# Kernel tuning notes

Measured on AMD Instinct MI355X. Metric: run time of the kernel, lower is better.

Reference implementation:

```python
import jax, jax.numpy as jnp
import numpy as np

B, V, D = 32768, 2, 512   # batch, views (code hard-codes 2 via cat(subject, subject)), hidden dim
S, L = 32, 8              # number of subjects, number of labels -> K = S*L groups
DENS_TEMP = 0.1           # args.Intersubsim_dens_temp (temperature/base_temperature are unused in forward)


def setup_inputs() -> dict:
    key = jax.random.key(0)
    k1, k2, k3 = jax.random.split(key, 3)
    X_data = jax.random.normal(k1, (B, V, D), dtype=jnp.float32)
    subject = jax.random.randint(k2, (B,), 0, S, dtype=jnp.int32)
    labels = jax.random.randint(k3, (B,), 0, L, dtype=jnp.int32)
    return {"X_data": X_data, "subject": subject, "labels": labels}


def reference(X_data, subject, labels):
    K = S * L
    # contrast_feature = cat(unbind(X_data, dim=1), dim=0): view-major stacking -> [V*B, D]
    feat = jnp.concatenate([X_data[:, v, :] for v in range(V)], axis=0)
    sub2 = jnp.concatenate([subject, subject])   # subject_ten
    lab2 = jnp.concatenate([labels, labels])     # labels_ten

    # group id per row; loop order (sorted unique subject, sorted unique label) == s*L + l
    gid = sub2 * L + lab2                         # [2B]
    counts = jax.ops.segment_sum(jnp.ones(gid.shape, feat.dtype), gid, K)   # [K]
    sums = jax.ops.segment_sum(feat, gid, K)                                 # [K, D]
    centroid = sums / counts[:, None]                                        # per-group mean

    # per-point euclidean distance to own-group centroid (torch.cdist)
    dist = jnp.sqrt(jnp.sum((feat - centroid[gid]) ** 2, axis=1))            # [2B]
    # density: mean(dist ** 0.5) / log(n_g + 10) for groups with >1 member
    mean_sqrt = jax.ops.segment_sum(jnp.sqrt(dist), gid, K) / counts
    dens = mean_sqrt / jnp.log(counts + 10.0)
    dmax = jnp.max(jnp.where(counts > 1, dens, -jnp.inf))
    density = jnp.where(counts > 1, dens, dmax)
    density = jnp.clip(density, jnp.quantile(density, 0.1), jnp.quantile(density, 0.9))
    density = DENS_TEMP * density / density.mean()
    # torch path goes through .tolist() -> density carries no gradient
    density = jax.lax.stop_gradient(density)

    # masks: positives = same label, different subject (group index equals raw id here)
    g_sub = jnp.arange(K, dtype=sub2.dtype) // L
    g_lab = jnp.arange(K, dtype=lab2.dtype) % L
    mask = ((sub2[:, None] != g_sub[None, :]) & (lab2[:, None] == g_lab[None, :])).astype(feat.dtype)  # [2B, K]
    # with S>=2 and all labels present, every row has at least one positive -> no row drop

    sim = (feat @ centroid.T) / density[None, :]          # [2B, K]
    sim = sim - jnp.max(sim, axis=1, keepdims=True)
    positive_sim = sim * mask
    # CrossEntropyLoss with soft (unnormalized) float targets: -sum target*log_softmax
    logp = jax.nn.log_softmax(positive_sim, axis=1)
    loss = -jnp.sum(mask * logp, axis=1) / jnp.sum(mask, axis=1)
    return loss.mean()
```

## Files before the change

### kernel.cpp

```cpp
#include <hip/hip_runtime.h>
#include <math.h>

#define BN 32768
#define DN 512
#define SN 32
#define LN 8
#define KN 256
#define N2 65536
#define SPLIT 8

typedef __attribute__((ext_vector_type(8))) short bf16x8;
typedef __attribute__((ext_vector_type(4))) float f32x4;

#define OFF_XBF     0ull
#define OFF_PART    67108864ull
#define OFF_SUMS    71303168ull
#define OFF_CENTB   71827456ull
#define OFF_GID     72089600ull
#define OFF_PERM    72220672ull
#define OFF_BASE    72351744ull
#define OFF_OFFW    72352772ull
#define OFF_COUNTS  72353796ull
#define OFF_SUMQ    72354820ull
#define OFF_INVD    72355844ull
#define OFF_LOSS    72356868ull
#define ZERO_OFF    OFF_COUNTS
#define ZERO_BYTES  (72356872ull - OFF_COUNTS)

__device__ __forceinline__ float atomAddF(float* p, float v) {
  return unsafeAtomicAdd(p, v);
}

__device__ __forceinline__ ushort f2bf(float x) {
  union { float f; unsigned u; } v; v.f = x;
  unsigned u = v.u;
  unsigned r = (u + 0x7fffu + ((u >> 16) & 1u)) >> 16;
  return (ushort)r;
}

__device__ __forceinline__ float bf2f(ushort x) {
  union { unsigned u; float f; } v; v.u = ((unsigned)x) << 16;
  return v.f;
}

__global__ __launch_bounds__(256) void k0_gid(const int* __restrict__ subject,
    const int* __restrict__ labels, int* __restrict__ gid, int* __restrict__ counts) {
  __shared__ int hist[KN];
  hist[threadIdx.x] = 0;
  __syncthreads();
  const int b0 = blockIdx.x * 1024;
  for (int i = threadIdx.x; i < 1024; i += 256) {
    int b = b0 + i;
    int g = subject[b] * LN + labels[b];
    gid[b] = g;
    atomicAdd(&hist[g], 1);
  }
  __syncthreads();
  if (hist[threadIdx.x]) atomicAdd(&counts[threadIdx.x], 2 * hist[threadIdx.x]);
}

__global__ __launch_bounds__(256) void k0b_scan(const int* __restrict__ counts,
    int* __restrict__ base, int* __restrict__ offw) {
  __shared__ int sh[KN];
  const int t = threadIdx.x;
  const int h = counts[t] >> 1;
  sh[t] = h;
  __syncthreads();
  for (int d = 1; d < 256; d <<= 1) {
    int add = (t >= d) ? sh[t - d] : 0;
    __syncthreads();
    sh[t] += add;
    __syncthreads();
  }
  const int excl = sh[t] - h;
  base[t] = excl;
  offw[t] = excl;
  if (t == 255) base[256] = sh[255];
}

__global__ __launch_bounds__(256) void k0c_scatter(const int* __restrict__ gid,
    int* __restrict__ offw, int* __restrict__ perm) {
  const int b = blockIdx.x * 256 + threadIdx.x;
  const int g = gid[b];
  const int pos = atomicAdd(&offw[g], 1);
  perm[pos] = b;
}

__global__ __launch_bounds__(256) void k1_sums(const float* __restrict__ X,
    const int* __restrict__ perm, const int* __restrict__ base,
    ushort* __restrict__ Xb, float* __restrict__ partial) {
  __shared__ float buf[512];
  const int g = blockIdx.x >> 3;
  const int s = blockIdx.x & (SPLIT - 1);
  const int t = threadIdx.x;
  const int start = base[g], end = base[g + 1];

  float4 acc = {0.f, 0.f, 0.f, 0.f};
  int i = start + s;
  if (i < end) {
    int idx = perm[i];
    float4 x = *(const float4*)(X + (size_t)idx * 1024 + t * 4);
    while (true) {
      const int inext = i + SPLIT;
      int idxn = idx;
      float4 xn = x;
      if (inext < end) {
        idxn = perm[inext];
        xn = *(const float4*)(X + (size_t)idxn * 1024 + t * 4);
      }
      acc.x += x.x; acc.y += x.y; acc.z += x.z; acc.w += x.w;
      ushort4 u = {f2bf(x.x), f2bf(x.y), f2bf(x.z), f2bf(x.w)};
      const size_t dst = (t < 128) ? ((size_t)idx * DN + t * 4)
                                   : ((size_t)(idx + BN) * DN + (t - 128) * 4);
      *(ushort4*)(Xb + dst) = u;
      if (inext >= end) break;
      i = inext; idx = idxn; x = xn;
    }
  }
  if (t >= 128) *(float4*)&buf[(t - 128) * 4] = acc;
  __syncthreads();
  if (t < 128) {
    float4 o = *(float4*)&buf[t * 4];
    float4 out = {acc.x + o.x, acc.y + o.y, acc.z + o.z, acc.w + o.w};
    *(float4*)&partial[((size_t)s * KN + g) * DN + t * 4] = out;
  }
}

__global__ __launch_bounds__(256) void k1b_cent(const float* __restrict__ partial,
    const int* __restrict__ counts, float* __restrict__ sums,
    ushort* __restrict__ centB) {
  const int i = blockIdx.x * 256 + threadIdx.x;
  const int g = i >> 9;
  float ss = 0.f;
#pragma unroll
  for (int s = 0; s < SPLIT; ++s) ss += partial[(size_t)s * (KN * DN) + i];
  sums[i] = ss;
  centB[i] = f2bf(ss / (float)counts[g]);
}

__global__ __launch_bounds__(256) void k3_dist(const ushort* __restrict__ Xb,
    const int* __restrict__ perm, const int* __restrict__ base,
    const float* __restrict__ sums, const int* __restrict__ counts,
    float* __restrict__ sumq) {
  __shared__ float wacc[4];
  const int g = blockIdx.x >> 3;
  const int s = blockIdx.x & (SPLIT - 1);
  const int t = threadIdx.x;
  const int w = t >> 6;
  const int lane = t & 63;
  const int start = base[g], end = base[g + 1];
  const int nviews = 2 * (end - start);
  const float invc = 1.0f / (float)counts[g];
  const float* sp = sums + g * DN + lane * 8;
  float4 c0 = *(const float4*)sp;
  float4 c1 = *(const float4*)(sp + 4);
  const float cs[8] = {c0.x * invc, c0.y * invc, c0.z * invc, c0.w * invc,
                       c1.x * invc, c1.y * invc, c1.z * invc, c1.w * invc};
  float q = 0.f;
  const int vs = s * 4 + w;
  for (int j = vs; j < nviews; j += SPLIT * 4) {
    const int idx = perm[start + (j >> 1)];
    const int row = idx + (j & 1) * BN;
    int4 chunk = *(const int4*)(Xb + (size_t)row * DN + lane * 8);
    const ushort* us = (const ushort*)&chunk;
    float ss = 0.f;
#pragma unroll
    for (int k = 0; k < 8; ++k) {
      float diff = bf2f(us[k]) - cs[k];
      ss += diff * diff;
    }
#pragma unroll
    for (int off = 32; off > 0; off >>= 1) ss += __shfl_down(ss, off, 64);
    if (lane == 0) q += sqrtf(sqrtf(ss));
  }
  if (lane == 0) wacc[w] = q;
  __syncthreads();
  if (t == 0) atomAddF(&sumq[g], wacc[0] + wacc[1] + wacc[2] + wacc[3]);
}

__global__ __launch_bounds__(256) void k4_density(const float* __restrict__ sumq,
    const int* __restrict__ counts, float* __restrict__ invd) {
  __shared__ float sv[256];
  __shared__ float st[256];
  const int t = threadIdx.x;
  const int cnt = counts[t];
  const bool valid = cnt > 1;
  float dens = 0.f;
  if (valid) dens = (sumq[t] / (float)cnt) / logf((float)cnt + 10.f);
  sv[t] = valid ? dens : -INFINITY;
  __syncthreads();
  for (int s = 128; s > 0; s >>= 1) {
    if (t < s) sv[t] = fmaxf(sv[t], sv[t + s]);
    __syncthreads();
  }
  const float dmax = sv[0];
  __syncthreads();
  const float d0 = valid ? dens : dmax;
  sv[t] = d0;
  __syncthreads();
  int rank = 0;
  for (int j = 0; j < 256; ++j) {
    float vj = sv[j];
    rank += (vj < d0) || (vj == d0 && j < t);
  }
  st[rank] = d0;
  __syncthreads();
  const float q10 = 0.5f * (st[25] + st[26]);
  const float q90 = 0.5f * (st[229] + st[230]);
  const float dc = fminf(fmaxf(d0, q10), q90);
  sv[t] = dc;
  __syncthreads();
  for (int s = 128; s > 0; s >>= 1) {
    if (t < s) sv[t] += sv[t + s];
    __syncthreads();
  }
  const float mean = sv[0] * (1.0f / 256.f);
  invd[t] = mean / (0.1f * dc);
}

#define ARS 144
#define BRS 144
__global__ __launch_bounds__(256, 2) void k5_mfma(const ushort* __restrict__ Xb,
    const ushort* __restrict__ centB, const int* __restrict__ subject,
    const int* __restrict__ labels, const float* __restrict__ invd,
    float* __restrict__ losssum) {
  __shared__ char smem[128 * ARS + 256 * BRS + 1024];
  char* ldsA = smem;
  char* ldsB = smem + 128 * ARS;
  float* maxbuf = (float*)smem;
  float* gmax = (float*)(smem + 2048);
  float* ebuf = (float*)(smem + 2560);
  float* zbuf = (float*)(smem + 4608);
  int* labs = (int*)(smem + 128 * ARS + 256 * BRS);
  int* subs = labs + 128;

  const int t = threadIdx.x;
  const int w = t >> 6;
  const int lane = t & 63;
  const int quad = lane >> 4;
  const int n16 = lane & 15;
  const int rowbase = blockIdx.x * 128;

  if (t < 128) {
    int b = (rowbase + t) & (BN - 1);
    labs[t] = labels[b];
    subs[t] = subject[b];
  }

  f32x4 acc[8][4];
#pragma unroll
  for (int mt = 0; mt < 8; ++mt)
#pragma unroll
    for (int nt = 0; nt < 4; ++nt) acc[mt][nt] = (f32x4){0.f, 0.f, 0.f, 0.f};

  const ushort* Arow = Xb + (size_t)rowbase * DN;

  for (int k0 = 0; k0 < DN; k0 += 64) {
    __syncthreads();
#pragma unroll
    for (int i = 0; i < 4; ++i) {
      int j = t + i * 256;
      int r = j >> 3, c = j & 7;
      *(int4*)(ldsA + r * ARS + c * 16) =
          *(const int4*)(Arow + (size_t)r * DN + k0 + c * 8);
    }
#pragma unroll
    for (int i = 0; i < 8; ++i) {
      int j = t + i * 256;
      int g = j >> 3, c = j & 7;
      *(int4*)(ldsB + g * BRS + c * 16) =
          *(const int4*)(centB + (size_t)g * DN + k0 + c * 8);
    }
    __syncthreads();
#pragma unroll
    for (int s = 0; s < 2; ++s) {
      bf16x8 bfr[4];
#pragma unroll
      for (int nt = 0; nt < 4; ++nt) {
        int g = w * 64 + nt * 16 + n16;
        bfr[nt] = *(bf16x8*)(ldsB + g * BRS + s * 64 + quad * 16);
      }
#pragma unroll
      for (int mt = 0; mt < 8; ++mt) {
        bf16x8 afr = *(bf16x8*)(ldsA + (mt * 16 + n16) * ARS + s * 64 + quad * 16);
#pragma unroll
        for (int nt = 0; nt < 4; ++nt)
          acc[mt][nt] = __builtin_amdgcn_mfma_f32_16x16x32_bf16(afr, bfr[nt], acc[mt][nt], 0, 0, 0);
      }
    }
  }

  float iv[4];
#pragma unroll
  for (int nt = 0; nt < 4; ++nt) iv[nt] = invd[w * 64 + nt * 16 + n16];

  __syncthreads();

#pragma unroll
  for (int mt = 0; mt < 8; ++mt) {
#pragma unroll
    for (int r = 0; r < 4; ++r) {
      float mm = -INFINITY;
#pragma unroll
      for (int nt = 0; nt < 4; ++nt) mm = fmaxf(mm, acc[mt][nt][r] * iv[nt]);
#pragma unroll
      for (int off = 1; off < 16; off <<= 1) mm = fmaxf(mm, __shfl_xor(mm, off, 64));
      if (n16 == 0) maxbuf[w * 128 + mt * 16 + quad * 4 + r] = mm;
    }
  }
  __syncthreads();
  if (t < 128)
    gmax[t] = fmaxf(fmaxf(maxbuf[t], maxbuf[128 + t]),
                    fmaxf(maxbuf[256 + t], maxbuf[384 + t]));
  __syncthreads();

#pragma unroll
  for (int mt = 0; mt < 8; ++mt) {
#pragma unroll
    for (int r = 0; r < 4; ++r) {
      const int row = mt * 16 + quad * 4 + r;
      const float gm = gmax[row];
      const int lab = labs[row];
      const int sub = subs[row];
      float e = 0.f, z = 0.f;
      if ((n16 & 7) == lab) {
#pragma unroll
        for (int nt = 0; nt < 4; ++nt) {
          int gdiv8 = w * 8 + nt * 2 + (n16 >> 3);
          if (gdiv8 != sub) {
            float sv = acc[mt][nt][r] * iv[nt] - gm;
            e += expf(sv);
            z += sv;
          }
        }
      }
#pragma unroll
      for (int off = 1; off < 16; off <<= 1) {
        e += __shfl_xor(e, off, 64);
        z += __shfl_xor(z, off, 64);
      }
      if (n16 == 0) {
        ebuf[w * 128 + row] = e;
        zbuf[w * 128 + row] = z;
      }
    }
  }
  __syncthreads();

  float lsum = 0.f;
  if (t < 128) {
    float e = ebuf[t] + ebuf[128 + t] + ebuf[256 + t] + ebuf[384 + t];
    float z = zbuf[t] + zbuf[128 + t] + zbuf[256 + t] + zbuf[384 + t];
    lsum = logf(225.f + e) - z * (1.0f / 31.0f);
  }
#pragma unroll
  for (int off = 32; off > 0; off >>= 1) lsum += __shfl_down(lsum, off, 64);
  if (lane == 0 && lsum != 0.f) atomAddF(losssum, lsum);
}

__global__ void k6_final(const float* __restrict__ losssum, float* __restrict__ out) {
  out[0] = losssum[0] * (1.0f / (float)N2);
}

extern "C" void kernel_launch(void* const* d_in, const int* in_sizes, int n_in,
                              void* d_out, int out_size, void* d_ws, size_t ws_size,
                              hipStream_t stream) {
  const float* X = (const float*)d_in[0];
  const int* subject = (const int*)d_in[1];
  const int* labels = (const int*)d_in[2];
  char* ws = (char*)d_ws;
  ushort* Xb = (ushort*)(ws + OFF_XBF);
  float* partial = (float*)(ws + OFF_PART);
  float* sums = (float*)(ws + OFF_SUMS);
  ushort* centB = (ushort*)(ws + OFF_CENTB);
  int* gid = (int*)(ws + OFF_GID);
  int* perm = (int*)(ws + OFF_PERM);
  int* basep = (int*)(ws + OFF_BASE);
  int* offw = (int*)(ws + OFF_OFFW);
  int* counts = (int*)(ws + OFF_COUNTS);
  float* sumq = (float*)(ws + OFF_SUMQ);
  float* invd = (float*)(ws + OFF_INVD);
  float* losssum = (float*)(ws + OFF_LOSS);

  hipMemsetAsync(ws + ZERO_OFF, 0, ZERO_BYTES, stream);
  k0_gid<<<BN / 1024, 256, 0, stream>>>(subject, labels, gid, counts);
  k0b_scan<<<1, 256, 0, stream>>>(counts, basep, offw);
  k0c_scatter<<<BN / 256, 256, 0, stream>>>(gid, offw, perm);
  k1_sums<<<KN * SPLIT, 256, 0, stream>>>(X, perm, basep, Xb, partial);
  k1b_cent<<<(KN * DN) / 256, 256, 0, stream>>>(partial, counts, sums, centB);
  k3_dist<<<KN * SPLIT, 256, 0, stream>>>(Xb, perm, basep, sums, counts, sumq);
  k4_density<<<1, 256, 0, stream>>>(sumq, counts, invd);
  k5_mfma<<<N2 / 128, 256, 0, stream>>>(Xb, centB, subject, labels, invd, losssum);
  k6_final<<<1, 1, 0, stream>>>(losssum, (float*)d_out);
}
```

Before: 314.1 us.

## Load MFMA tiles via direct global-to-LDS async loads with XOR swizzle

Replaces register-staged int4 copies into padded LDS tiles with global_load_lds direct-to-LDS 16-byte loads. To avoid bank conflicts without padding, it uses an XOR swizzle of the 16-byte chunk index by row, applied both when loading and when reading fragments. This removes VGPR round-trips and shrinks LDS footprint. It risks correctness if the LDS address semantics of global_load_lds (wave-uniform base plus lane offset) do not match the assumed layout, and no waitcnt for vmcnt is explicitly issued before the barrier.

```diff
diff --git a/kernel.cpp b/kernel.cpp
--- a/kernel.cpp
+++ b/kernel.cpp
@@ -41,6 +41,12 @@
 __device__ __forceinline__ float bf2f(ushort x) {
   union { unsigned u; float f; } v; v.u = ((unsigned)x) << 16;
   return v.f;
+}
+
+__device__ __forceinline__ void async16(const void* g, void* l) {
+  __builtin_amdgcn_global_load_lds(
+      (const __attribute__((address_space(1))) unsigned int*)g,
+      (__attribute__((address_space(3))) unsigned int*)l, 16, 0, 0);
 }
 
 __global__ __launch_bounds__(256) void k0_gid(const int* __restrict__ subject,
@@ -218,20 +224,20 @@
   invd[t] = mean / (0.1f * dc);
 }
 
-#define ARS 144
-#define BRS 144
+#define TAB (128 * 128)
+#define TBB (256 * 128)
 __global__ __launch_bounds__(256, 2) void k5_mfma(const ushort* __restrict__ Xb,
     const ushort* __restrict__ centB, const int* __restrict__ subject,
     const int* __restrict__ labels, const float* __restrict__ invd,
     float* __restrict__ losssum) {
-  __shared__ char smem[128 * ARS + 256 * BRS + 1024];
+  __shared__ char smem[TAB + TBB + 1024];
   char* ldsA = smem;
-  char* ldsB = smem + 128 * ARS;
+  char* ldsB = smem + TAB;
   float* maxbuf = (float*)smem;
   float* gmax = (float*)(smem + 2048);
   float* ebuf = (float*)(smem + 2560);
   float* zbuf = (float*)(smem + 4608);
-  int* labs = (int*)(smem + 128 * ARS + 256 * BRS);
+  int* labs = (int*)(smem + TAB + TBB);
   int* subs = labs + 128;
 
   const int t = threadIdx.x;
@@ -239,6 +245,9 @@
   const int lane = t & 63;
   const int quad = lane >> 4;
   const int n16 = lane & 15;
+  const int li = lane >> 3;
+  const int lc = lane & 7;
+  const int srcc = lc ^ li;
   const int rowbase = blockIdx.x * 128;
 
   if (t < 128) {
@@ -258,31 +267,28 @@
   for (int k0 = 0; k0 < DN; k0 += 64) {
     __syncthreads();
 #pragma unroll
-    for (int i = 0; i < 4; ++i) {
-      int j = t + i * 256;
-      int r = j >> 3, c = j & 7;
-      *(int4*)(ldsA + r * ARS + c * 16) =
-          *(const int4*)(Arow + (size_t)r * DN + k0 + c * 8);
-    }
-#pragma unroll
-    for (int i = 0; i < 8; ++i) {
-      int j = t + i * 256;
-      int g = j >> 3, c = j & 7;
-      *(int4*)(ldsB + g * BRS + c * 16) =
-          *(const int4*)(centB + (size_t)g * DN + k0 + c * 8);
+    for (int q = 0; q < 4; ++q) {
+      const int r0 = w * 32 + q * 8;
+      async16(Arow + (size_t)(r0 + li) * DN + k0 + srcc * 8, ldsA + r0 * 128);
+    }
+#pragma unroll
+    for (int q = 0; q < 8; ++q) {
+      const int g0 = w * 64 + q * 8;
+      async16(centB + (size_t)(g0 + li) * DN + k0 + srcc * 8, ldsB + g0 * 128);
     }
     __syncthreads();
 #pragma unroll
     for (int s = 0; s < 2; ++s) {
+      const int csw = ((s * 4 + quad) ^ (n16 & 7)) * 16;
       bf16x8 bfr[4];
 #pragma unroll
       for (int nt = 0; nt < 4; ++nt) {
         int g = w * 64 + nt * 16 + n16;
-        bfr[nt] = *(bf16x8*)(ldsB + g * BRS + s * 64 + quad * 16);
+        bfr[nt] = *(bf16x8*)(ldsB + g * 128 + csw);
       }
 #pragma unroll
       for (int mt = 0; mt < 8; ++mt) {
-        bf16x8 afr = *(bf16x8*)(ldsA + (mt * 16 + n16) * ARS + s * 64 + quad * 16);
+        bf16x8 afr = *(bf16x8*)(ldsA + (mt * 16 + n16) * 128 + csw);
 #pragma unroll
         for (int nt = 0; nt < 4; ++nt)
           acc[mt][nt] = __builtin_amdgcn_mfma_f32_16x16x32_bf16(afr, bfr[nt], acc[mt][nt], 0, 0, 0);
```

New measurement: 313.0 us. Within noise of the previous version (-0.4%).
